# Kernel tuning notes

Hardware: AMD Instinct MI355X
Metric: run time of the kernel (lower is better)

The kernel has to match this reference:

```python
import jax, jax.numpy as jnp
import numpy as np

STRIDE = 32
ANCHOR_SCALES = (16, 32, 64)
RATIOS = (0.5, 1.0, 2.0)
BASE_SIZE = 16
A = 9                    # base_anchors
PRE_NMS_TOP_N = 6000
POST_NMS_TOP_N = 1000
NMS_THRESH = 0.7
MIN_SIZE = 16.0


def _base_anchors():
    w = h = float(BASE_SIZE)
    cx = cy = (BASE_SIZE - 1) * 0.5
    out = []
    for r in RATIOS:
        ws = np.round(np.sqrt(w * h / r))
        hs = np.round(ws * r)
        for s in ANCHOR_SCALES:
            W_, H_ = ws * s, hs * s
            out.append([cx - 0.5 * (W_ - 1), cy - 0.5 * (H_ - 1),
                        cx + 0.5 * (W_ - 1), cy + 0.5 * (H_ - 1)])
    return np.asarray(out, dtype=np.float32)  # [9,4]


def _conv(x, w, b, padding):
    y = jax.lax.conv_general_dilated(x, w, (1, 1), padding,
                                     dimension_numbers=('NCHW', 'OIHW', 'NCHW'))
    return y + b[None, :, None, None]


def reference(features, rpn_w, rpn_b, cls_w, cls_b, box_w, box_b, image_height, image_width):
    H, W = features.shape[2], features.shape[3]
    x = jax.nn.relu(_conv(features, rpn_w, rpn_b, 'SAME'))
    cls_score = _conv(x, cls_w, cls_b, 'VALID')           # [1,2A,H,W]
    cls_prob = jax.nn.softmax(cls_score, axis=1)           # nn.Softmax2d: softmax over all 2A channels
    bbox_pred = _conv(x, box_w, box_b, 'VALID')            # [1,4A,H,W]

    scores = cls_prob[0, A:].transpose(1, 2, 0).reshape(-1)       # fg scores [H*W*A]
    deltas = bbox_pred[0].transpose(1, 2, 0).reshape(-1, 4)        # [H*W*A,4]

    base = jnp.asarray(_base_anchors())
    sx = jnp.arange(W, dtype=jnp.float32) * STRIDE
    sy = jnp.arange(H, dtype=jnp.float32) * STRIDE
    sxx, syy = jnp.meshgrid(sx, sy)                                # [H,W]
    shifts = jnp.stack([sxx, syy, sxx, syy], axis=-1).reshape(-1, 4)
    anchors = (shifts[:, None, :] + base[None, :, :]).reshape(-1, 4)

    # bbox_transform_inv decode
    wa = anchors[:, 2] - anchors[:, 0] + 1.0
    ha = anchors[:, 3] - anchors[:, 1] + 1.0
    cxa = anchors[:, 0] + 0.5 * (wa - 1.0)
    cya = anchors[:, 1] + 0.5 * (ha - 1.0)
    cx = deltas[:, 0] * wa + cxa
    cy = deltas[:, 1] * ha + cya
    pw = wa * jnp.exp(deltas[:, 2])
    ph = ha * jnp.exp(deltas[:, 3])
    x1 = jnp.clip(cx - 0.5 * pw, 0.0, image_width - 1.0)
    y1 = jnp.clip(cy - 0.5 * ph, 0.0, image_height - 1.0)
    x2 = jnp.clip(cx + 0.5 * pw, 0.0, image_width - 1.0)
    y2 = jnp.clip(cy + 0.5 * ph, 0.0, image_height - 1.0)
    boxes = jnp.stack([x1, y1, x2, y2], axis=-1)

    valid0 = ((x2 - x1 + 1.0) >= MIN_SIZE) & ((y2 - y1 + 1.0) >= MIN_SIZE)
    scores = jnp.where(valid0, scores, -jnp.inf)

    top_scores, top_idx = jax.lax.top_k(scores, PRE_NMS_TOP_N)
    tb = boxes[top_idx]                                             # [P,4]
    tx1, ty1, tx2, ty2 = tb[:, 0], tb[:, 1], tb[:, 2], tb[:, 3]
    areas = (tx2 - tx1 + 1.0) * (ty2 - ty1 + 1.0)
    xx1 = jnp.maximum(tx1[:, None], tx1[None, :])
    yy1 = jnp.maximum(ty1[:, None], ty1[None, :])
    xx2 = jnp.minimum(tx2[:, None], tx2[None, :])
    yy2 = jnp.minimum(ty2[:, None], ty2[None, :])
    inter = jnp.maximum(xx2 - xx1 + 1.0, 0.0) * jnp.maximum(yy2 - yy1 + 1.0, 0.0)
    iou = inter / (areas[:, None] + areas[None, :] - inter)         # [P,P]

    def step(state, _):
        alive, = (state,) if not isinstance(state, tuple) else (None,)
        return state, None

    def nms_step(state, _):
        alive, sel_list = state
        s = jnp.where(alive, top_scores, -jnp.inf)
        j = jnp.argmax(s)
        ok = s[j] > -jnp.inf
        alive = alive & (jnp.take(iou, j, axis=0) <= NMS_THRESH)    # suppresses j too (iou=1)
        return (alive, sel_list), (j.astype(jnp.int32), ok)

    alive0 = jnp.isfinite(top_scores)
    (_, _), (sel, selv) = jax.lax.scan(nms_step, (alive0, 0),
                                       jnp.arange(POST_NMS_TOP_N), length=POST_NMS_TOP_N)

    out_boxes = tb[sel] * selv[:, None].astype(tb.dtype)            # zero-pad invalid slots
    rois = jnp.concatenate([jnp.zeros((POST_NMS_TOP_N, 1), tb.dtype), out_boxes], axis=1)
    return rois                                                     # [POST_NMS_TOP_N, 5]


def setup_inputs() -> dict:
    key = jax.random.key(0)
    ks = jax.random.split(key, 4)
    features = jax.random.normal(ks[0], (1, 256, 128, 128), dtype=jnp.float32)
    rpn_w = 0.01 * jax.random.normal(ks[1], (256, 256, 3, 3), dtype=jnp.float32)
    rpn_b = jnp.zeros((256,), jnp.float32)
    cls_w = 0.01 * jax.random.normal(ks[2], (18, 256, 1, 1), dtype=jnp.float32)
    cls_b = jnp.zeros((18,), jnp.float32)
    box_w = 0.01 * jax.random.normal(ks[3], (36, 256, 1, 1), dtype=jnp.float32)
    box_b = jnp.zeros((36,), jnp.float32)
    return {'features': features, 'rpn_w': rpn_w, 'rpn_b': rpn_b,
            'cls_w': cls_w, 'cls_b': cls_b, 'box_w': box_w, 'box_b': box_b,
            'image_height': 4096, 'image_width': 4096}
```

## Files before the change

### kernel.cpp

```cpp
#include <hip/hip_runtime.h>
#include <stdint.h>
#include <math.h>

typedef unsigned long long u64;
typedef unsigned int u32;
typedef float float4a __attribute__((ext_vector_type(4), aligned(4)));

static const size_t OFF_CTL   = 0;
static const size_t OFF_HIST  = 1024;
static const size_t OFF_DOTS  = 1049600;
static const size_t OFF_WCV   = 4588544;
static const size_t OFF_XD    = 6947840;
static const size_t OFF_BOX   = 23725056;
static const size_t OFF_KEYS  = 26084352;
static const size_t OFF_CKEY  = 27264000;
static const size_t OFF_CIDX  = 27313152;
static const size_t OFF_TB    = 27337728;
static const size_t OFF_TSC   = 27433728;
static const size_t OFF_ALIVE = 27458048;
static const size_t OFF_MASK  = 27459072;
static const size_t OFF_FPAD  = 32067584;

__device__ __forceinline__ float exp_xla(float x) {
    float m = floorf(__fmaf_rn(x, 1.44269504088896341f, 0.5f));
    float r = __fmaf_rn(m, -0.693359375f, x);
    r = __fmaf_rn(m, 2.12194440e-4f, r);
    float r2 = r * r;
    float p = 1.9875691500e-4f;
    p = __fmaf_rn(p, r, 1.3981999507e-3f);
    p = __fmaf_rn(p, r, 8.3334519073e-3f);
    p = __fmaf_rn(p, r, 4.1665795894e-2f);
    p = __fmaf_rn(p, r, 1.6666665459e-1f);
    p = __fmaf_rn(p, r, 5.0000001201e-1f);
    p = __fmaf_rn(p, r2, r);
    p = __fadd_rn(p, 1.0f);
    int mi = (int)m;
    return p * __int_as_float((mi + 127) << 23);
}

__device__ __forceinline__ void gload_lds16(const void* g, void* l) {
    __builtin_amdgcn_global_load_lds(
        (const __attribute__((address_space(1))) void*)g,
        (__attribute__((address_space(3))) void*)l, 16, 0, 0);
}

__global__ void prep_wcv(const float* __restrict__ rpn_w, float* __restrict__ wcv) {
    int t = blockIdx.x * 256 + threadIdx.x;
    if (t >= 589824) return;
    int tap = t / 65536, rem = t % 65536, ic = rem / 256, oc = rem % 256;
    wcv[t] = rpn_w[oc * 2304 + ic * 9 + tap];
}

__global__ void prep_pad(const float* __restrict__ feat, float* __restrict__ featP) {
    int t = blockIdx.x * 256 + threadIdx.x;
    if (t >= 256 * 130 * 132) return;
    int ic = t / 17160, rem = t % 17160, y = rem / 132, x = rem % 132;
    int sy = y - 1, sx = x - 1;
    float v = 0.f;
    if (sy >= 0 && sy < 128 && sx >= 0 && sx < 128)
        v = feat[ic * 16384 + sy * 128 + sx];
    featP[t] = v;
}

__global__ __launch_bounds__(256, 2) void conv3x3(const float* __restrict__ featP,
                                                  const float* __restrict__ wcv,
                                                  const float* __restrict__ rpn_b,
                                                  float* __restrict__ xd) {
    __shared__ float sW[8192];
    const int band = blockIdx.x & 7;
    const int slot = blockIdx.x >> 3;
    const int tx = slot & 7, ocb = slot >> 3;
    const int oc0 = ocb * 32;
    const int tid = threadIdx.x;
    const int wid = tid >> 6;
    const int lane = tid & 63;
    const int py = lane >> 2, px0 = (lane & 3) * 4;
    const int gy = band * 16 + py, gx0 = tx * 16 + px0;
    const int ocB = oc0 + wid * 8;
    float acc[4][8];
#pragma unroll
    for (int p = 0; p < 4; ++p)
#pragma unroll
        for (int o = 0; o < 8; ++o) acc[p][o] = 0.f;
#pragma unroll
    for (int tap = 0; tap < 9; ++tap) {
        __syncthreads();
        for (int idx = tid; idx < 8192; idx += 256)
            sW[idx] = wcv[tap * 65536 + (idx >> 5) * 256 + oc0 + (idx & 31)];
        __syncthreads();
        const float* fp = featP + (size_t)(gy + tap / 3) * 132 + (gx0 + tap % 3);
        const float* wl = sW + wid * 8;
#pragma unroll 4
        for (int ic = 0; ic < 256; ++ic) {
            float4a fA = *(const float4a*)(fp + (size_t)ic * 17160);
            float4a w0 = *(const float4a*)(wl + ic * 32);
            float4a w1 = *(const float4a*)(wl + ic * 32 + 4);
#pragma unroll
            for (int p = 0; p < 4; ++p) {
#pragma unroll
                for (int o = 0; o < 4; ++o)
                    acc[p][o] = __fmaf_rn(fA[p], w0[o], acc[p][o]);
#pragma unroll
                for (int o = 0; o < 4; ++o)
                    acc[p][4 + o] = __fmaf_rn(fA[p], w1[o], acc[p][4 + o]);
            }
        }
    }
#pragma unroll
    for (int p = 0; p < 4; ++p) {
        float* op = xd + (size_t)(gy * 128 + gx0 + p) * 256 + ocB;
#pragma unroll
        for (int o = 0; o < 8; ++o) {
            float v = __fadd_rn(acc[p][o], rpn_b[ocB + o]);
            op[o] = v > 0.f ? v : 0.f;
        }
    }
}

__global__ __launch_bounds__(256, 1) void heads_seq(const float* __restrict__ xd,
                                                    const float* __restrict__ cls_w,
                                                    const float* __restrict__ box_w,
                                                    float* __restrict__ dots) {
    __shared__ float sX[4][260];
    const int tid = threadIdx.x;
    const int pix0 = blockIdx.x * 4;
    for (int idx = tid; idx < 1024; idx += 256)
        sX[idx >> 8][idx & 255] = xd[(size_t)(pix0 + (idx >> 8)) * 256 + (idx & 255)];
    __syncthreads();
    if (tid < 216) {
        const int pl = tid / 54, o = tid % 54;
        const float* wr = (o < 18) ? (cls_w + o * 256) : (box_w + (o - 18) * 256);
        const float4* x4 = (const float4*)&sX[pl][0];
        const float4* w4 = (const float4*)wr;
        float acc = 0.f;
        for (int q = 0; q < 64; ++q) {
            float4 xv = x4[q];
            float4 wv = w4[q];
            acc = __fmaf_rn(xv.x, wv.x, acc);
            acc = __fmaf_rn(xv.y, wv.y, acc);
            acc = __fmaf_rn(xv.z, wv.z, acc);
            acc = __fmaf_rn(xv.w, wv.w, acc);
        }
        dots[(size_t)(pix0 + pl) * 54 + o] = acc;
    }
}

__global__ __launch_bounds__(256, 1) void decode(const float* __restrict__ dots,
                                                 const float* __restrict__ cls_b,
                                                 const float* __restrict__ box_b,
                                                 float4* __restrict__ boxes,
                                                 u64* __restrict__ keys) {
    const int pix = blockIdx.x * 256 + threadIdx.x;
    if (pix >= 16384) return;
    const float* dt = dots + (size_t)pix * 54;
    float d[54];
#pragma unroll
    for (int i = 0; i < 54; ++i)
        d[i] = __fadd_rn(dt[i], (i < 18 ? cls_b[i] : box_b[i - 18]));
    float m = d[0];
#pragma unroll
    for (int i = 1; i < 18; ++i) m = fmaxf(m, d[i]);
    float e[18];
#pragma unroll
    for (int i = 0; i < 18; ++i) e[i] = exp_xla(__fsub_rn(d[i], m));
    float s = e[0];
#pragma unroll
    for (int i = 1; i < 18; ++i) s = __fadd_rn(s, e[i]);
    const int y = pix >> 7, x = pix & 127;
    const float shx = (float)(x * 32), shy = (float)(y * 32);
    const float AW[9] = {368.f, 736.f, 1472.f, 256.f, 512.f, 1024.f, 176.f, 352.f, 704.f};
    const float AH[9] = {192.f, 384.f, 768.f, 256.f, 512.f, 1024.f, 352.f, 704.f, 1408.f};
#pragma unroll
    for (int a = 0; a < 9; ++a) {
        float score = e[9 + a] / s;
        float wa = AW[a], ha = AH[a];
        float cxa = __fadd_rn(shx, 7.5f), cya = __fadd_rn(shy, 7.5f);
        float dx = d[18 + 4 * a], dyy = d[19 + 4 * a];
        float dw = d[20 + 4 * a], dh = d[21 + 4 * a];
        float cx = __fadd_rn(__fmul_rn(dx, wa), cxa);
        float cy = __fadd_rn(__fmul_rn(dyy, ha), cya);
        float pw = __fmul_rn(wa, exp_xla(dw));
        float ph = __fmul_rn(ha, exp_xla(dh));
        float hx = __fmul_rn(0.5f, pw), hy = __fmul_rn(0.5f, ph);
        float x1 = fminf(fmaxf(__fsub_rn(cx, hx), 0.f), 4095.f);
        float y1 = fminf(fmaxf(__fsub_rn(cy, hy), 0.f), 4095.f);
        float x2 = fminf(fmaxf(__fadd_rn(cx, hx), 0.f), 4095.f);
        float y2 = fminf(fmaxf(__fadd_rn(cy, hy), 0.f), 4095.f);
        float vw = __fadd_rn(__fsub_rn(x2, x1), 1.0f);
        float vh = __fadd_rn(__fsub_rn(y2, y1), 1.0f);
        bool valid = (vw >= 16.0f) && (vh >= 16.0f);
        int i = pix * 9 + a;
        boxes[i] = make_float4(x1, y1, x2, y2);
        u64 k;
        if (valid) {
            u32 b = __float_as_uint(score);
            k = ((u64)(u32)~(b | 0x80000000u) << 32) | (u32)i;
        } else {
            k = (0xFFFFFFFFULL << 32) | (u32)i;
        }
        keys[i] = k;
    }
}

__global__ __launch_bounds__(256) void hist8(const u64* __restrict__ keys,
                                             u32* __restrict__ ghist,
                                             const u64* __restrict__ pfx, int pass) {
    __shared__ u32 lh[256];
    lh[threadIdx.x] = 0;
    __syncthreads();
    const u64 pref = *pfx;
    const int shift = 56 - 8 * pass;
    for (int i = blockIdx.x * 256 + threadIdx.x; i < 147456; i += 64 * 256) {
        u64 k = keys[i];
        bool match = (pass == 0) || ((k >> (shift + 8)) == pref);
        if (match) atomicAdd(&lh[(u32)(k >> shift) & 0xFFu], 1u);
    }
    __syncthreads();
    if (lh[threadIdx.x]) atomicAdd(&ghist[threadIdx.x], lh[threadIdx.x]);
}

__global__ __launch_bounds__(256) void scan8(const u32* __restrict__ ghist,
                                             u64* pfx, u32* tgt, int pass) {
    __shared__ u32 h[256];
    __shared__ u32 incl[256];
    const int t = threadIdx.x;
    u32 target = (pass == 0) ? 6000u : *tgt;
    u64 p0 = (pass == 0) ? 0ULL : *pfx;
    h[t] = ghist[t];
    incl[t] = h[t];
    __syncthreads();
    for (int off = 1; off < 256; off <<= 1) {
        u32 v = (t >= off) ? incl[t - off] : 0u;
        __syncthreads();
        incl[t] += v;
        __syncthreads();
    }
    u32 before = incl[t] - h[t];
    if (before < target && target <= incl[t]) {
        *pfx = (p0 << 8) | (u64)t;
        *tgt = target - before;
    }
}

__global__ void compact(const u64* __restrict__ keys, const u64* __restrict__ kstar,
                        u32* count, u64* __restrict__ ckey, u32* __restrict__ cidx) {
    int i = blockIdx.x * 256 + threadIdx.x;
    if (i >= 147456) return;
    u64 k = keys[i];
    if (k <= *kstar) {
        u32 pos = atomicAdd(count, 1u);
        if (pos < 6144) { ckey[pos] = k; cidx[pos] = (u32)(k & 0xFFFFFFFFu); }
    }
}

__global__ __launch_bounds__(256) void rank_scatter(const u64* __restrict__ ckey,
                                                    const u32* __restrict__ cidx,
                                                    const u32* __restrict__ count,
                                                    const float4* __restrict__ boxes,
                                                    float4* __restrict__ tb,
                                                    float* __restrict__ tsc) {
    __shared__ u64 LK[6144];
    int N = (int)*count; if (N > 6144) N = 6144;
    for (int i = threadIdx.x; i < N; i += 256) LK[i] = ckey[i];
    __syncthreads();
    int e = blockIdx.x * 256 + threadIdx.x;
    if (e >= N) return;
    u64 myK = LK[e];
    u32 myI = cidx[e];
    int rank = 0;
    for (int c = 0; c < N; ++c) rank += (LK[c] < myK);
    if (rank < 6000) {
        tb[rank] = boxes[myI];
        u32 hi = (u32)(myK >> 32);
        tsc[rank] = (hi == 0xFFFFFFFFu) ? -__builtin_inff()
                                        : __uint_as_float(~hi & 0x7FFFFFFFu);
    }
}

__global__ void alive_init(const float* __restrict__ tsc, u64* __restrict__ alive0) {
    int r = blockIdx.x * 256 + threadIdx.x;
    bool a = false;
    if (r < 6000) a = tsc[r] > -__builtin_inff();
    u64 b = __ballot(a);
    if ((threadIdx.x & 63) == 0) alive0[r >> 6] = b;
}

__global__ __launch_bounds__(256) void nms_mask(const float4* __restrict__ tb,
                                                u64* __restrict__ mask) {
    int tid = blockIdx.x * 256 + threadIdx.x;
    if (tid >= 6000 * 94) return;
    int j = tid / 94, w = tid % 94;
    float4 bj = tb[j];
    float arJ = __fmul_rn(__fadd_rn(__fsub_rn(bj.z, bj.x), 1.0f),
                          __fadd_rn(__fsub_rn(bj.w, bj.y), 1.0f));
    u64 m = 0;
    int base = w * 64;
#pragma unroll 4
    for (int b = 0; b < 64; ++b) {
        int i = base + b;
        if (i >= 6000) break;
        float4 bi = tb[i];
        float arI = __fmul_rn(__fadd_rn(__fsub_rn(bi.z, bi.x), 1.0f),
                              __fadd_rn(__fsub_rn(bi.w, bi.y), 1.0f));
        float xx1 = fmaxf(bj.x, bi.x), yy1 = fmaxf(bj.y, bi.y);
        float xx2 = fminf(bj.z, bi.z), yy2 = fminf(bj.w, bi.w);
        float ww = fmaxf(__fadd_rn(__fsub_rn(xx2, xx1), 1.0f), 0.0f);
        float hh = fmaxf(__fadd_rn(__fsub_rn(yy2, yy1), 1.0f), 0.0f);
        float inter = __fmul_rn(ww, hh);
        float uni = __fsub_rn(__fadd_rn(arJ, arI), inter);
        float iou = inter / uni;
        if (iou > 0.7f) m |= (1ULL << b);
    }
    mask[(size_t)j * 96 + w] = m;
}

__global__ __launch_bounds__(64, 1) void nms_seq(const u64* __restrict__ alive0,
                                                 const u64* __restrict__ mask,
                                                 const float4* __restrict__ tb,
                                                 float* __restrict__ out) {
    __shared__ __align__(16) u64 lwin[64 * 96];
    __shared__ u32 sel[1000];
    const int lane = threadIdx.x;
    u64 wl = alive0[lane];
    u64 wh = (lane < 30) ? alive0[64 + lane] : 0ULL;
    int base = -1000000;
    int k = 0;
    for (; k < 1000; ++k) {
        int j;
        {
            u64 blo = __ballot(wl != 0ULL);
            if (blo) {
                int l = __ffsll((long long)blo) - 1;
                u64 w = __shfl(wl, l);
                j = l * 64 + __ffsll((long long)w) - 1;
            } else {
                u64 bhi = __ballot(wh != 0ULL);
                if (!bhi) break;
                int l = __ffsll((long long)bhi) - 1;
                u64 w = __shfl(wh, l);
                j = (64 + l) * 64 + __ffsll((long long)w) - 1;
            }
        }
        if (lane == 0) sel[k] = (u32)j;
        int s = j - base;
        if (s < 0 || s >= 64) {
            const char* gsrc = (const char*)mask + (size_t)j * 768 + (size_t)lane * 16;
            char* ldst = (char*)lwin;
#pragma unroll
            for (int i = 0; i < 48; ++i)
                gload_lds16(gsrc + (size_t)i * 1024, ldst + i * 1024);
            base = j;
            s = 0;
            asm volatile("s_waitcnt vmcnt(0)" ::: "memory");
        }
        u64 rl = lwin[(size_t)s * 96 + lane];
        u64 rh = (lane < 30) ? lwin[(size_t)s * 96 + 64 + lane] : 0ULL;
        wl &= ~rl;
        if (lane < 30) wh &= ~rh;
    }
    __syncthreads();
    for (int r = lane; r < k; r += 64) {
        int j = (int)sel[r];
        float4 bj = tb[j];
        out[r * 5 + 1] = bj.x;
        out[r * 5 + 2] = bj.y;
        out[r * 5 + 3] = bj.z;
        out[r * 5 + 4] = bj.w;
    }
}

extern "C" void kernel_launch(void* const* d_in, const int* in_sizes, int n_in,
                              void* d_out, int out_size, void* d_ws, size_t ws_size,
                              hipStream_t stream) {
    const float *feat = nullptr, *rpn_w = nullptr, *rpn_b = nullptr;
    const float *cls_w = nullptr, *cls_b = nullptr, *box_w = nullptr, *box_b = nullptr;
    for (int i = 0; i < n_in; ++i) {
        switch (in_sizes[i]) {
            case 4194304: feat  = (const float*)d_in[i]; break;
            case 589824:  rpn_w = (const float*)d_in[i]; break;
            case 256:     rpn_b = (const float*)d_in[i]; break;
            case 4608:    cls_w = (const float*)d_in[i]; break;
            case 18:      cls_b = (const float*)d_in[i]; break;
            case 9216:    box_w = (const float*)d_in[i]; break;
            case 36:      box_b = (const float*)d_in[i]; break;
            default: break;
        }
    }

    char* w = (char*)d_ws;
    u64* pfx       = (u64*)(w + OFF_CTL);
    u32* tgt       = (u32*)(w + OFF_CTL + 8);
    u32* ctlCount  = (u32*)(w + OFF_CTL + 12);
    u32* hist      = (u32*)(w + OFF_HIST);
    float* dots    = (float*)(w + OFF_DOTS);
    float* wcv     = (float*)(w + OFF_WCV);
    float* xd      = (float*)(w + OFF_XD);
    float4* boxes  = (float4*)(w + OFF_BOX);
    u64* keys      = (u64*)(w + OFF_KEYS);
    u64* ckey      = (u64*)(w + OFF_CKEY);
    u32* cidx      = (u32*)(w + OFF_CIDX);
    float4* tb     = (float4*)(w + OFF_TB);
    float* tsc     = (float*)(w + OFF_TSC);
    u64* alive0    = (u64*)(w + OFF_ALIVE);
    u64* mask      = (u64*)(w + OFF_MASK);
    float* featP   = (float*)(w + OFF_FPAD);

    hipMemsetAsync(d_ws, 0, OFF_HIST + 8 * 256 * 4, stream);
    hipMemsetAsync(d_out, 0, (size_t)out_size * sizeof(float), stream);

    prep_wcv<<<2304, 256, 0, stream>>>(rpn_w, wcv);
    prep_pad<<<17160, 256, 0, stream>>>(feat, featP);
    conv3x3<<<512, 256, 0, stream>>>(featP, wcv, rpn_b, xd);
    heads_seq<<<4096, 256, 0, stream>>>(xd, cls_w, box_w, dots);
    decode<<<64, 256, 0, stream>>>(dots, cls_b, box_b, boxes, keys);
    for (int p = 0; p < 8; ++p) {
        hist8<<<64, 256, 0, stream>>>(keys, hist + p * 256, pfx, p);
        scan8<<<1, 256, 0, stream>>>(hist + p * 256, pfx, tgt, p);
    }
    compact<<<576, 256, 0, stream>>>(keys, pfx, ctlCount, ckey, cidx);
    rank_scatter<<<24, 256, 0, stream>>>(ckey, cidx, ctlCount, boxes, tb, tsc);
    alive_init<<<24, 256, 0, stream>>>(tsc, alive0);
    nms_mask<<<2204, 256, 0, stream>>>(tb, mask);
    nms_seq<<<1, 64, 0, stream>>>(alive0, mask, tb, (float*)d_out);
}
```

Measured before the change: 936.4 us.

## Widen conv3x3 output-channel tile and double-buffer NMS mask window prefetch

The conv3x3 kernel now computes 64 output channels per block (16 per wave) instead of 32, so each feature load is reused across twice as many FMAs. It loads the weights into LDS with vectorized float4 copies and launches half as many blocks. The NMS sequential loop double-buffers the 64-row mask window, prefetching the next window asynchronously while the current one is consumed, and uses readlane instead of shfl for the 64-bit broadcast. The risks are higher register pressure (64 accumulators, launch bounds lowered to 1) and only 256 blocks for the conv, which may underfill the GPU.

```diff
diff --git a/kernel.cpp b/kernel.cpp
--- a/kernel.cpp
+++ b/kernel.cpp
@@ -62,39 +62,44 @@
     featP[t] = v;
 }
 
-__global__ __launch_bounds__(256, 2) void conv3x3(const float* __restrict__ featP,
+__global__ __launch_bounds__(256, 1) void conv3x3(const float* __restrict__ featP,
                                                   const float* __restrict__ wcv,
                                                   const float* __restrict__ rpn_b,
                                                   float* __restrict__ xd) {
-    __shared__ float sW[8192];
+    __shared__ float sW[16384];
     const int band = blockIdx.x & 7;
-    const int slot = blockIdx.x >> 3;
-    const int tx = slot & 7, ocb = slot >> 3;
-    const int oc0 = ocb * 32;
+    const int tx = (blockIdx.x >> 3) & 7;
+    const int ocb = blockIdx.x >> 6;
+    const int oc0 = ocb * 64;
     const int tid = threadIdx.x;
     const int wid = tid >> 6;
     const int lane = tid & 63;
     const int py = lane >> 2, px0 = (lane & 3) * 4;
     const int gy = band * 16 + py, gx0 = tx * 16 + px0;
-    const int ocB = oc0 + wid * 8;
-    float acc[4][8];
+    const int ocB = oc0 + wid * 16;
+    float acc[4][16];
 #pragma unroll
     for (int p = 0; p < 4; ++p)
 #pragma unroll
-        for (int o = 0; o < 8; ++o) acc[p][o] = 0.f;
+        for (int o = 0; o < 16; ++o) acc[p][o] = 0.f;
 #pragma unroll
     for (int tap = 0; tap < 9; ++tap) {
         __syncthreads();
-        for (int idx = tid; idx < 8192; idx += 256)
-            sW[idx] = wcv[tap * 65536 + (idx >> 5) * 256 + oc0 + (idx & 31)];
+        for (int idx = tid; idx < 4096; idx += 256) {
+            int ic = idx >> 4, oq = idx & 15;
+            *(float4a*)&sW[ic * 64 + oq * 4] =
+                *(const float4a*)&wcv[tap * 65536 + ic * 256 + oc0 + oq * 4];
+        }
         __syncthreads();
         const float* fp = featP + (size_t)(gy + tap / 3) * 132 + (gx0 + tap % 3);
-        const float* wl = sW + wid * 8;
-#pragma unroll 4
+        const float* wl = sW + wid * 16;
+#pragma unroll 8
         for (int ic = 0; ic < 256; ++ic) {
             float4a fA = *(const float4a*)(fp + (size_t)ic * 17160);
-            float4a w0 = *(const float4a*)(wl + ic * 32);
-            float4a w1 = *(const float4a*)(wl + ic * 32 + 4);
+            float4a w0 = *(const float4a*)(wl + ic * 64);
+            float4a w1 = *(const float4a*)(wl + ic * 64 + 4);
+            float4a w2 = *(const float4a*)(wl + ic * 64 + 8);
+            float4a w3 = *(const float4a*)(wl + ic * 64 + 12);
 #pragma unroll
             for (int p = 0; p < 4; ++p) {
 #pragma unroll
@@ -103,6 +108,12 @@
 #pragma unroll
                 for (int o = 0; o < 4; ++o)
                     acc[p][4 + o] = __fmaf_rn(fA[p], w1[o], acc[p][4 + o]);
+#pragma unroll
+                for (int o = 0; o < 4; ++o)
+                    acc[p][8 + o] = __fmaf_rn(fA[p], w2[o], acc[p][8 + o]);
+#pragma unroll
+                for (int o = 0; o < 4; ++o)
+                    acc[p][12 + o] = __fmaf_rn(fA[p], w3[o], acc[p][12 + o]);
             }
         }
     }
@@ -110,7 +121,7 @@
     for (int p = 0; p < 4; ++p) {
         float* op = xd + (size_t)(gy * 128 + gx0 + p) * 256 + ocB;
 #pragma unroll
-        for (int o = 0; o < 8; ++o) {
+        for (int o = 0; o < 16; ++o) {
             float v = __fadd_rn(acc[p][o], rpn_b[ocB + o]);
             op[o] = v > 0.f ? v : 0.f;
         }
@@ -318,12 +329,14 @@
                                                  const u64* __restrict__ mask,
                                                  const float4* __restrict__ tb,
                                                  float* __restrict__ out) {
-    __shared__ __align__(16) u64 lwin[64 * 96];
+    __shared__ __align__(16) u64 lwin[2][64 * 96];
     __shared__ u32 sel[1000];
     const int lane = threadIdx.x;
     u64 wl = alive0[lane];
     u64 wh = (lane < 30) ? alive0[64 + lane] : 0ULL;
     int base = -1000000;
+    int pbase = -1;
+    int cur = 0;
     int k = 0;
     for (; k < 1000; ++k) {
         int j;
@@ -331,30 +344,49 @@
             u64 blo = __ballot(wl != 0ULL);
             if (blo) {
                 int l = __ffsll((long long)blo) - 1;
-                u64 w = __shfl(wl, l);
+                u32 a = __builtin_amdgcn_readlane((u32)wl, l);
+                u32 b = __builtin_amdgcn_readlane((u32)(wl >> 32), l);
+                u64 w = ((u64)b << 32) | (u64)a;
                 j = l * 64 + __ffsll((long long)w) - 1;
             } else {
                 u64 bhi = __ballot(wh != 0ULL);
                 if (!bhi) break;
                 int l = __ffsll((long long)bhi) - 1;
-                u64 w = __shfl(wh, l);
+                u32 a = __builtin_amdgcn_readlane((u32)wh, l);
+                u32 b = __builtin_amdgcn_readlane((u32)(wh >> 32), l);
+                u64 w = ((u64)b << 32) | (u64)a;
                 j = (64 + l) * 64 + __ffsll((long long)w) - 1;
             }
         }
         if (lane == 0) sel[k] = (u32)j;
-        int s = j - base;
-        if (s < 0 || s >= 64) {
-            const char* gsrc = (const char*)mask + (size_t)j * 768 + (size_t)lane * 16;
-            char* ldst = (char*)lwin;
-#pragma unroll
-            for (int i = 0; i < 48; ++i)
-                gload_lds16(gsrc + (size_t)i * 1024, ldst + i * 1024);
-            base = j;
-            s = 0;
-            asm volatile("s_waitcnt vmcnt(0)" ::: "memory");
-        }
-        u64 rl = lwin[(size_t)s * 96 + lane];
-        u64 rh = (lane < 30) ? lwin[(size_t)s * 96 + 64 + lane] : 0ULL;
+        if (j >= base + 64) {
+            if (pbase >= 0 && j < pbase + 64) {
+                asm volatile("s_waitcnt vmcnt(0)" ::: "memory");
+                cur ^= 1;
+                base = pbase;
+            } else {
+                asm volatile("s_waitcnt vmcnt(0)" ::: "memory");
+                const char* gsrc = (const char*)mask + (size_t)j * 768 + (size_t)lane * 16;
+                char* ldst = (char*)&lwin[cur][0];
+#pragma unroll
+                for (int i = 0; i < 48; ++i)
+                    gload_lds16(gsrc + (size_t)i * 1024, ldst + i * 1024);
+                base = j;
+                asm volatile("s_waitcnt vmcnt(0)" ::: "memory");
+            }
+            pbase = -1;
+            if (base + 64 < 6000) {
+                const char* gs2 = (const char*)mask + (size_t)(base + 64) * 768 + (size_t)lane * 16;
+                char* ld2 = (char*)&lwin[cur ^ 1][0];
+#pragma unroll
+                for (int i = 0; i < 48; ++i)
+                    gload_lds16(gs2 + (size_t)i * 1024, ld2 + i * 1024);
+                pbase = base + 64;
+            }
+        }
+        const int s = j - base;
+        u64 rl = lwin[cur][(size_t)s * 96 + lane];
+        u64 rh = (lane < 30) ? lwin[cur][(size_t)s * 96 + 64 + lane] : 0ULL;
         wl &= ~rl;
         if (lane < 30) wh &= ~rh;
     }
@@ -410,7 +442,7 @@
 
     prep_wcv<<<2304, 256, 0, stream>>>(rpn_w, wcv);
     prep_pad<<<17160, 256, 0, stream>>>(feat, featP);
-    conv3x3<<<512, 256, 0, stream>>>(featP, wcv, rpn_b, xd);
+    conv3x3<<<256, 256, 0, stream>>>(featP, wcv, rpn_b, xd);
     heads_seq<<<4096, 256, 0, stream>>>(xd, cls_w, box_w, dots);
     decode<<<64, 256, 0, stream>>>(dots, cls_b, box_b, boxes, keys);
     for (int p = 0; p < 8; ++p) {
```

Result: no change. 932.0 us (-0.5%).

## Double-buffer NMS mask windows in LDS with prefetch of next window

Applied to the files above, without the earlier changes.

The sequential NMS kernel now keeps two LDS windows of suppression-mask rows. Whenever it loads a window, it also starts an asynchronous load of the next 64 rows, so later window switches can skip a full synchronous global-to-LDS stall. It also replaces the 64-bit shuffle with two scalar readlanes to pick the first alive word. This doubles LDS use and makes the window bookkeeping more complex, and the clamping of window starts near the end of the mask needs to stay correct.

```diff
diff --git a/kernel.cpp b/kernel.cpp
--- a/kernel.cpp
+++ b/kernel.cpp
@@ -318,12 +318,14 @@
                                                  const u64* __restrict__ mask,
                                                  const float4* __restrict__ tb,
                                                  float* __restrict__ out) {
-    __shared__ __align__(16) u64 lwin[64 * 96];
+    __shared__ __align__(16) u64 lwin[2][64 * 96];
     __shared__ u32 sel[1000];
     const int lane = threadIdx.x;
     u64 wl = alive0[lane];
     u64 wh = (lane < 30) ? alive0[64 + lane] : 0ULL;
     int base = -1000000;
+    int pbase = -1;
+    int cur = 0;
     int k = 0;
     for (; k < 1000; ++k) {
         int j;
@@ -331,30 +333,51 @@
             u64 blo = __ballot(wl != 0ULL);
             if (blo) {
                 int l = __ffsll((long long)blo) - 1;
-                u64 w = __shfl(wl, l);
+                u32 a = __builtin_amdgcn_readlane((u32)wl, l);
+                u32 b = __builtin_amdgcn_readlane((u32)(wl >> 32), l);
+                u64 w = ((u64)b << 32) | (u64)a;
                 j = l * 64 + __ffsll((long long)w) - 1;
             } else {
                 u64 bhi = __ballot(wh != 0ULL);
                 if (!bhi) break;
                 int l = __ffsll((long long)bhi) - 1;
-                u64 w = __shfl(wh, l);
+                u32 a = __builtin_amdgcn_readlane((u32)wh, l);
+                u32 b = __builtin_amdgcn_readlane((u32)(wh >> 32), l);
+                u64 w = ((u64)b << 32) | (u64)a;
                 j = (64 + l) * 64 + __ffsll((long long)w) - 1;
             }
         }
         if (lane == 0) sel[k] = (u32)j;
-        int s = j - base;
-        if (s < 0 || s >= 64) {
-            const char* gsrc = (const char*)mask + (size_t)j * 768 + (size_t)lane * 16;
-            char* ldst = (char*)lwin;
-#pragma unroll
-            for (int i = 0; i < 48; ++i)
-                gload_lds16(gsrc + (size_t)i * 1024, ldst + i * 1024);
-            base = j;
-            s = 0;
-            asm volatile("s_waitcnt vmcnt(0)" ::: "memory");
-        }
-        u64 rl = lwin[(size_t)s * 96 + lane];
-        u64 rh = (lane < 30) ? lwin[(size_t)s * 96 + 64 + lane] : 0ULL;
+        if (j >= base + 64) {
+            if (pbase >= 0 && j < pbase + 64) {
+                asm volatile("s_waitcnt vmcnt(0)" ::: "memory");
+                cur ^= 1;
+                base = pbase;
+            } else {
+                int js = (j > 5936) ? 5936 : j;
+                asm volatile("s_waitcnt vmcnt(0)" ::: "memory");
+                const char* gsrc = (const char*)mask + (size_t)js * 768 + (size_t)lane * 16;
+                char* ldst = (char*)&lwin[cur][0];
+#pragma unroll
+                for (int i = 0; i < 48; ++i)
+                    gload_lds16(gsrc + (size_t)i * 1024, ldst + i * 1024);
+                base = js;
+                asm volatile("s_waitcnt vmcnt(0)" ::: "memory");
+            }
+            pbase = -1;
+            if (base + 64 < 6000) {
+                int ps = (base + 64 > 5936) ? 5936 : (base + 64);
+                const char* gs2 = (const char*)mask + (size_t)ps * 768 + (size_t)lane * 16;
+                char* ld2 = (char*)&lwin[cur ^ 1][0];
+#pragma unroll
+                for (int i = 0; i < 48; ++i)
+                    gload_lds16(gs2 + (size_t)i * 1024, ld2 + i * 1024);
+                pbase = ps;
+            }
+        }
+        const int s = j - base;
+        u64 rl = lwin[cur][(size_t)s * 96 + lane];
+        u64 rh = (lane < 30) ? lwin[cur][(size_t)s * 96 + 64 + lane] : 0ULL;
         wl &= ~rl;
         if (lane < 30) wh &= ~rh;
     }
```

Result: faster. 912.4 us (-2.6%).
